# Kernel tuning notes

Measured on AMD Instinct MI355X. Metric: run time of the kernel, lower is better.

The kernel has to match this reference:

```python
import jax, jax.numpy as jnp
import numpy as np

E = 512
H = 8
D = E // H  # 64
B = 2
S = 4096


def setup_inputs() -> dict:
    key = jax.random.key(0)
    ks = jax.random.split(key, 12)
    s = 1.0 / np.sqrt(E)
    return {
        "x": jax.random.normal(ks[0], (B, S, E), dtype=jnp.float32),
        "bias": jax.random.normal(ks[1], (H, 1, S, S), dtype=jnp.float32),
        "mask": jax.random.randint(ks[2], (1, 1, S, S), 0, 2, dtype=jnp.int32),
        "Wq": jax.random.normal(ks[3], (E, E), dtype=jnp.float32) * s,
        "bq": jnp.zeros((E,), dtype=jnp.float32),
        "Wk": jax.random.normal(ks[4], (E, E), dtype=jnp.float32) * s,
        "bk": jnp.zeros((E,), dtype=jnp.float32),
        "Wv": jax.random.normal(ks[5], (E, E), dtype=jnp.float32) * s,
        "bv": jnp.zeros((E,), dtype=jnp.float32),
        "Wo": jax.random.normal(ks[6], (E, E), dtype=jnp.float32) * s,
        "bo": jnp.zeros((E,), dtype=jnp.float32),
    }


def _split_heads(t):
    # [B,S,E] -> [H,B,S,D]  (matches x.view(B,-1,H,D).permute(2,0,1,3))
    b, s, _ = t.shape
    return t.reshape(b, s, H, D).transpose(2, 0, 1, 3)


def reference(x, bias, mask, Wq, bq, Wk, bk, Wv, bv, Wo, bo):
    # torch Linear: y = x @ W.T + b
    q = _split_heads(x @ Wq.T + bq)  # [H,B,S,D]
    k = _split_heads(x @ Wk.T + bk)
    v = _split_heads(x @ Wv.T + bv)

    scores = jnp.einsum("hbqd,hbkd->hbqk", q, k) + bias  # [H,B,S,S]
    scores = jnp.where(mask == 0, jnp.float32(-1e20), scores)
    # NOTE: original divides AFTER bias-add and masking
    probs = jax.nn.softmax(scores / jnp.sqrt(jnp.float32(D)), axis=-1)
    out = jnp.einsum("hbqk,hbkd->hbqd", probs, v)  # [H,B,S,D]
    out = out.transpose(1, 2, 0, 3).reshape(x.shape[0], -1, H * D)  # [B,S,E]
    return out @ Wo.T + bo
```

## Files before the change

kernel.cpp:

```cpp
#include <hip/hip_runtime.h>
#include <hip/hip_bf16.h>

typedef __bf16 bf16x8 __attribute__((ext_vector_type(8)));
typedef float f32x4 __attribute__((ext_vector_type(4)));

#define S_LEN 4096
#define EMB   512
#define NHEAD 8
#define HDIM  64
#define NBAT  2
#define NROW  (NBAT * S_LEN)

static __device__ __forceinline__ f32x4 mfma16x16(bf16x8 a, bf16x8 b, f32x4 c) {
    return __builtin_amdgcn_mfma_f32_16x16x32_bf16(a, b, c, 0, 0, 0);
}

__global__ __launch_bounds__(256) void convert_kernel(
    const float* __restrict__ x, const float* __restrict__ Wq,
    const float* __restrict__ Wk, const float* __restrict__ Wv,
    const float* __restrict__ Wo,
    __hip_bfloat16* __restrict__ xb, __hip_bfloat16* __restrict__ wqkv,
    __hip_bfloat16* __restrict__ wob)
{
    const int NX = NROW * EMB;
    const int NW = EMB * EMB;
    int i = blockIdx.x * 256 + threadIdx.x;
    if (i < NX) { xb[i] = __float2bfloat16(x[i]); return; }
    int j = i - NX;
    if (j < 3 * NW) {
        int p = j >> 18, r = j & (NW - 1);
        const float* src = (p == 0) ? Wq : (p == 1) ? Wk : Wv;
        wqkv[j] = __float2bfloat16(src[r]);
    } else if (j < 4 * NW) {
        int r = j - 3 * NW;
        wob[r] = __float2bfloat16(Wo[r]);
    }
}

__device__ __forceinline__ void gemm_core(
    const __hip_bfloat16* __restrict__ A, const __hip_bfloat16* __restrict__ Bw,
    int mbase, int nbase,
    __hip_bfloat16* As, __hip_bfloat16* Bs, f32x4 acc[2][4])
{
    const int tid = threadIdx.x;
    const int w = tid >> 6, lane = tid & 63, l = lane & 15, quad = lane >> 4;
    const f32x4 zero = {0.f, 0.f, 0.f, 0.f};
#pragma unroll
    for (int mb = 0; mb < 2; mb++)
#pragma unroll
        for (int nb = 0; nb < 4; nb++) acc[mb][nb] = zero;

    for (int k0 = 0; k0 < EMB; k0 += 32) {
        __syncthreads();
#pragma unroll
        for (int c = tid; c < 512; c += 256) {
            int row = c >> 2, kc = c & 3;
            uint4 v = *(const uint4*)(A + (size_t)(mbase + row) * EMB + k0 + kc * 8);
            *(uint4*)(As + row * 40 + kc * 8) = v;
        }
        {
            int row = tid >> 2, kc = tid & 3;
            uint4 v = *(const uint4*)(Bw + (size_t)(nbase + row) * EMB + k0 + kc * 8);
            *(uint4*)(Bs + row * 40 + kc * 8) = v;
        }
        __syncthreads();

        bf16x8 af[2], bfr[4];
#pragma unroll
        for (int mb = 0; mb < 2; mb++)
            af[mb] = *(const bf16x8*)(As + (w * 32 + mb * 16 + l) * 40 + quad * 8);
#pragma unroll
        for (int nb = 0; nb < 4; nb++)
            bfr[nb] = *(const bf16x8*)(Bs + (nb * 16 + l) * 40 + quad * 8);
#pragma unroll
        for (int mb = 0; mb < 2; mb++)
#pragma unroll
            for (int nb = 0; nb < 4; nb++)
                acc[mb][nb] = mfma16x16(af[mb], bfr[nb], acc[mb][nb]);
    }
}

__global__ __launch_bounds__(256, 4) void qkv_gemm(
    const __hip_bfloat16* __restrict__ xb, const __hip_bfloat16* __restrict__ wqkv,
    const float* __restrict__ bq, const float* __restrict__ bk, const float* __restrict__ bv,
    __hip_bfloat16* __restrict__ Qh, __hip_bfloat16* __restrict__ Kh,
    __hip_bfloat16* __restrict__ Vt)
{
    __shared__ __align__(16) __hip_bfloat16 As[128 * 40];
    __shared__ __align__(16) __hip_bfloat16 Bs[64 * 40];
    const int mbase = blockIdx.x * 128, nbase = blockIdx.y * 64;
    f32x4 acc[2][4];
    gemm_core(xb, wqkv, mbase, nbase, As, Bs, acc);

    const int tid = threadIdx.x;
    const int w = tid >> 6, lane = tid & 63, l = lane & 15, quad = lane >> 4;
    const int p = nbase >> 9;
    const float* bias = (p == 0) ? bq : (p == 1) ? bk : bv;
    __hip_bfloat16* dst = (p == 0) ? Qh : (p == 1) ? Kh : Vt;
#pragma unroll
    for (int mb = 0; mb < 2; mb++)
#pragma unroll
        for (int nb = 0; nb < 4; nb++)
#pragma unroll
            for (int r = 0; r < 4; r++) {
                int m = mbase + w * 32 + mb * 16 + quad * 4 + r;
                int n = nbase + nb * 16 + l;
                int o = n & 511;
                float v = acc[mb][nb][r] + bias[o];
                int b = m >> 12, s = m & 4095, hh = o >> 6, d = o & 63;
                size_t idx = (p == 2)
                    ? ((size_t)((hh * 2 + b) * 64 + d)) * 4096 + s
                    : ((size_t)((hh * 2 + b) * 4096 + s)) * 64 + d;
                dst[idx] = __float2bfloat16(v);
            }
}

__global__ __launch_bounds__(256, 2) void attn_kernel(
    const __hip_bfloat16* __restrict__ Qh, const __hip_bfloat16* __restrict__ Kh,
    const __hip_bfloat16* __restrict__ Vt,
    const float* __restrict__ bias, const int* __restrict__ mask,
    __hip_bfloat16* __restrict__ Om)
{
    const int h = blockIdx.y, qt = blockIdx.x;
    const int tid = threadIdx.x;
    const int w = tid >> 6, lane = tid & 63, l = lane & 15, quad = lane >> 4;
    const int q0 = qt * 64;
    const float CS = 0.18033688011112042f;

    __shared__ __align__(16) __hip_bfloat16 Ks[2][64 * 72];
    __shared__ __align__(16) __hip_bfloat16 Vs[2][64 * 72];
    __shared__ __align__(16) __hip_bfloat16 Ps[64 * 72];

    bf16x8 qf[2][2];
#pragma unroll
    for (int b = 0; b < 2; b++) {
        const __hip_bfloat16* qp =
            Qh + ((size_t)((h * 2 + b) * 4096 + q0 + w * 16 + l)) * 64;
        qf[b][0] = *(const bf16x8*)(qp + quad * 8);
        qf[b][1] = *(const bf16x8*)(qp + 32 + quad * 8);
    }

    f32x4 oacc[2][4];
    float mst[2][4], lst[2][4];
    const f32x4 zero = {0.f, 0.f, 0.f, 0.f};
#pragma unroll
    for (int b = 0; b < 2; b++) {
#pragma unroll
        for (int nb = 0; nb < 4; nb++) oacc[b][nb] = zero;
#pragma unroll
        for (int r = 0; r < 4; r++) { mst[b][r] = -__builtin_inff(); lst[b][r] = 0.f; }
    }

    for (int kt = 0; kt < 64; kt++) {
        const int k0 = kt * 64;
        __syncthreads();
#pragma unroll
        for (int c = tid; c < 2048; c += 256) {
            int t = c >> 9;
            int b = t & 1, isV = t >> 1;
            int cc = c & 511, row = cc >> 3, ch = cc & 7;
            const __hip_bfloat16* src = isV
                ? Vt + ((size_t)((h * 2 + b) * 64 + row)) * 4096 + k0 + ch * 8
                : Kh + ((size_t)((h * 2 + b) * 4096 + k0 + row)) * 64 + ch * 8;
            uint4 v = *(const uint4*)src;
            *(uint4*)((isV ? Vs[b] : Ks[b]) + row * 72 + ch * 8) = v;
        }
        float bor[4][4];
#pragma unroll
        for (int nb = 0; nb < 4; nb++)
#pragma unroll
            for (int r = 0; r < 4; r++) {
                int qq = q0 + w * 16 + quad * 4 + r;
                int kk = k0 + nb * 16 + l;
                float bb = bias[(size_t)h * S_LEN * S_LEN + (size_t)qq * S_LEN + kk];
                int mm = mask[(size_t)qq * S_LEN + kk];
                bor[nb][r] = mm ? bb : -1e30f;
            }
        __syncthreads();

#pragma unroll
        for (int b = 0; b < 2; b++) {
            f32x4 sc[4] = {zero, zero, zero, zero};
#pragma unroll
            for (int ks = 0; ks < 2; ks++)
#pragma unroll
                for (int nb = 0; nb < 4; nb++) {
                    bf16x8 kf = *(const bf16x8*)(Ks[b] + (nb * 16 + l) * 72 + ks * 32 + quad * 8);
                    sc[nb] = mfma16x16(qf[b][ks], kf, sc[nb]);
                }
            float xv[4][4], rmax[4];
#pragma unroll
            for (int r = 0; r < 4; r++) rmax[r] = -__builtin_inff();
#pragma unroll
            for (int nb = 0; nb < 4; nb++)
#pragma unroll
                for (int r = 0; r < 4; r++) {
                    xv[nb][r] = (sc[nb][r] + bor[nb][r]) * CS;
                    rmax[r] = fmaxf(rmax[r], xv[nb][r]);
                }
#pragma unroll
            for (int r = 0; r < 4; r++) {
                rmax[r] = fmaxf(rmax[r], __shfl_xor(rmax[r], 1));
                rmax[r] = fmaxf(rmax[r], __shfl_xor(rmax[r], 2));
                rmax[r] = fmaxf(rmax[r], __shfl_xor(rmax[r], 4));
                rmax[r] = fmaxf(rmax[r], __shfl_xor(rmax[r], 8));
            }
            float alpha[4], rsum[4];
#pragma unroll
            for (int r = 0; r < 4; r++) {
                float mn = fmaxf(mst[b][r], rmax[r]);
                alpha[r] = __builtin_amdgcn_exp2f(mst[b][r] - mn);
                mst[b][r] = mn;
                rsum[r] = 0.f;
            }
            float pv[4][4];
#pragma unroll
            for (int nb = 0; nb < 4; nb++)
#pragma unroll
                for (int r = 0; r < 4; r++) {
                    float e = __builtin_amdgcn_exp2f(xv[nb][r] - mst[b][r]);
                    pv[nb][r] = e;
                    rsum[r] += e;
                }
#pragma unroll
            for (int r = 0; r < 4; r++) {
                rsum[r] += __shfl_xor(rsum[r], 1);
                rsum[r] += __shfl_xor(rsum[r], 2);
                rsum[r] += __shfl_xor(rsum[r], 4);
                rsum[r] += __shfl_xor(rsum[r], 8);
                lst[b][r] = lst[b][r] * alpha[r] + rsum[r];
            }
#pragma unroll
            for (int nb = 0; nb < 4; nb++)
#pragma unroll
                for (int r = 0; r < 4; r++) oacc[b][nb][r] *= alpha[r];
#pragma unroll
            for (int nb = 0; nb < 4; nb++)
#pragma unroll
                for (int r = 0; r < 4; r++)
                    Ps[(w * 16 + quad * 4 + r) * 72 + nb * 16 + l] =
                        __float2bfloat16(pv[nb][r]);
#pragma unroll
            for (int ks = 0; ks < 2; ks++) {
                bf16x8 pf = *(const bf16x8*)(Ps + (w * 16 + l) * 72 + ks * 32 + quad * 8);
#pragma unroll
                for (int nb = 0; nb < 4; nb++) {
                    bf16x8 vf = *(const bf16x8*)(Vs[b] + (nb * 16 + l) * 72 + ks * 32 + quad * 8);
                    oacc[b][nb] = mfma16x16(pf, vf, oacc[b][nb]);
                }
            }
        }
    }

#pragma unroll
    for (int b = 0; b < 2; b++)
#pragma unroll
        for (int nb = 0; nb < 4; nb++)
#pragma unroll
            for (int r = 0; r < 4; r++) {
                int qq = q0 + w * 16 + quad * 4 + r;
                float val = oacc[b][nb][r] / lst[b][r];
                Om[((size_t)(b * 4096 + qq)) * 512 + h * 64 + nb * 16 + l] =
                    __float2bfloat16(val);
            }
}

__global__ __launch_bounds__(256, 4) void out_gemm(
    const __hip_bfloat16* __restrict__ Om, const __hip_bfloat16* __restrict__ wob,
    const float* __restrict__ bo, float* __restrict__ out)
{
    __shared__ __align__(16) __hip_bfloat16 As[128 * 40];
    __shared__ __align__(16) __hip_bfloat16 Bs[64 * 40];
    const int mbase = blockIdx.x * 128, nbase = blockIdx.y * 64;
    f32x4 acc[2][4];
    gemm_core(Om, wob, mbase, nbase, As, Bs, acc);

    const int tid = threadIdx.x;
    const int w = tid >> 6, lane = tid & 63, l = lane & 15, quad = lane >> 4;
#pragma unroll
    for (int mb = 0; mb < 2; mb++)
#pragma unroll
        for (int nb = 0; nb < 4; nb++)
#pragma unroll
            for (int r = 0; r < 4; r++) {
                int m = mbase + w * 32 + mb * 16 + quad * 4 + r;
                int n = nbase + nb * 16 + l;
                out[(size_t)m * EMB + n] = acc[mb][nb][r] + bo[n];
            }
}

extern "C" void kernel_launch(void* const* d_in, const int* in_sizes, int n_in,
                              void* d_out, int out_size, void* d_ws, size_t ws_size,
                              hipStream_t stream) {
    const float* x    = (const float*)d_in[0];
    const float* bias = (const float*)d_in[1];
    const int*   mask = (const int*)d_in[2];
    const float* Wq   = (const float*)d_in[3];
    const float* bq   = (const float*)d_in[4];
    const float* Wk   = (const float*)d_in[5];
    const float* bk   = (const float*)d_in[6];
    const float* Wv   = (const float*)d_in[7];
    const float* bv   = (const float*)d_in[8];
    const float* Wo   = (const float*)d_in[9];
    const float* bo   = (const float*)d_in[10];
    float* out = (float*)d_out;

    char* ws = (char*)d_ws;
    __hip_bfloat16* xb   = (__hip_bfloat16*)ws; ws += (size_t)NROW * EMB * 2;
    __hip_bfloat16* wqkv = (__hip_bfloat16*)ws; ws += (size_t)3 * EMB * EMB * 2;
    __hip_bfloat16* wob  = (__hip_bfloat16*)ws; ws += (size_t)EMB * EMB * 2;
    __hip_bfloat16* Qh   = (__hip_bfloat16*)ws; ws += (size_t)NROW * EMB * 2;
    __hip_bfloat16* Kh   = (__hip_bfloat16*)ws; ws += (size_t)NROW * EMB * 2;
    __hip_bfloat16* Vt   = (__hip_bfloat16*)ws; ws += (size_t)NROW * EMB * 2;
    __hip_bfloat16* Om   = (__hip_bfloat16*)ws; ws += (size_t)NROW * EMB * 2;

    convert_kernel<<<dim3(20480), dim3(256), 0, stream>>>(
        x, Wq, Wk, Wv, Wo, xb, wqkv, wob);
    qkv_gemm<<<dim3(64, 24), dim3(256), 0, stream>>>(
        xb, wqkv, bq, bk, bv, Qh, Kh, Vt);
    attn_kernel<<<dim3(64, NHEAD), dim3(256), 0, stream>>>(
        Qh, Kh, Vt, bias, mask, Om);
    out_gemm<<<dim3(64, 8), dim3(256), 0, stream>>>(Om, wob, bo, out);
}
```

Measured before the change: 1.316 ms.

## Prefetch next K/V, bias and mask tiles into registers and raise MFMA priority

Result: faster. 1.261 ms (-4.1%).

```diff
diff --git a/kernel.cpp b/kernel.cpp
--- a/kernel.cpp
+++ b/kernel.cpp
@@ -50,21 +50,26 @@
 #pragma unroll
         for (int nb = 0; nb < 4; nb++) acc[mb][nb] = zero;
 
+    const int r0 = tid >> 2, kc = tid & 3;
+    const __hip_bfloat16* pa0 = A + (size_t)(mbase + r0) * EMB + kc * 8;
+    const __hip_bfloat16* pa1 = pa0 + (size_t)64 * EMB;
+    const __hip_bfloat16* pb  = Bw + (size_t)(nbase + r0) * EMB + kc * 8;
+
+    uint4 va0 = *(const uint4*)pa0;
+    uint4 va1 = *(const uint4*)pa1;
+    uint4 vb  = *(const uint4*)pb;
+
     for (int k0 = 0; k0 < EMB; k0 += 32) {
         __syncthreads();
-#pragma unroll
-        for (int c = tid; c < 512; c += 256) {
-            int row = c >> 2, kc = c & 3;
-            uint4 v = *(const uint4*)(A + (size_t)(mbase + row) * EMB + k0 + kc * 8);
-            *(uint4*)(As + row * 40 + kc * 8) = v;
-        }
-        {
-            int row = tid >> 2, kc = tid & 3;
-            uint4 v = *(const uint4*)(Bw + (size_t)(nbase + row) * EMB + k0 + kc * 8);
-            *(uint4*)(Bs + row * 40 + kc * 8) = v;
-        }
+        *(uint4*)(As + r0 * 40 + kc * 8)        = va0;
+        *(uint4*)(As + (r0 + 64) * 40 + kc * 8) = va1;
+        *(uint4*)(Bs + r0 * 40 + kc * 8)        = vb;
         __syncthreads();
-
+        if (k0 + 32 < EMB) {
+            va0 = *(const uint4*)(pa0 + k0 + 32);
+            va1 = *(const uint4*)(pa1 + k0 + 32);
+            vb  = *(const uint4*)(pb  + k0 + 32);
+        }
         bf16x8 af[2], bfr[4];
 #pragma unroll
         for (int mb = 0; mb < 2; mb++)
@@ -72,11 +77,13 @@
 #pragma unroll
         for (int nb = 0; nb < 4; nb++)
             bfr[nb] = *(const bf16x8*)(Bs + (nb * 16 + l) * 40 + quad * 8);
+        __builtin_amdgcn_s_setprio(1);
 #pragma unroll
         for (int mb = 0; mb < 2; mb++)
 #pragma unroll
             for (int nb = 0; nb < 4; nb++)
                 acc[mb][nb] = mfma16x16(af[mb], bfr[nb], acc[mb][nb]);
+        __builtin_amdgcn_s_setprio(0);
     }
 }
 
@@ -121,7 +128,7 @@
     const float* __restrict__ bias, const int* __restrict__ mask,
     __hip_bfloat16* __restrict__ Om)
 {
-    const int h = blockIdx.y, qt = blockIdx.x;
+    const int h = blockIdx.x, qt = blockIdx.y;
     const int tid = threadIdx.x;
     const int w = tid >> 6, lane = tid & 63, l = lane & 15, quad = lane >> 4;
     const int q0 = qt * 64;
@@ -151,36 +158,81 @@
         for (int r = 0; r < 4; r++) { mst[b][r] = -__builtin_inff(); lst[b][r] = 0.f; }
     }
 
+    const __hip_bfloat16* kvsrc[8];
+    __hip_bfloat16* kvdst[8];
+#pragma unroll
+    for (int j = 0; j < 8; j++) {
+        int c = j * 256 + tid;
+        int t = c >> 9, b = t & 1, isV = t >> 1;
+        int cc = c & 511, row = cc >> 3, ch = cc & 7;
+        if (isV) {
+            kvsrc[j] = Vt + ((size_t)((h * 2 + b) * 64 + row)) * 4096 + ch * 8;
+            kvdst[j] = Vs[b] + row * 72 + ch * 8;
+        } else {
+            kvsrc[j] = Kh + ((size_t)((h * 2 + b) * 4096 + row)) * 64 + ch * 8;
+            kvdst[j] = Ks[b] + row * 72 + ch * 8;
+        }
+    }
+    const float* bptr[4];
+    const int*   mptr[4];
+#pragma unroll
+    for (int r = 0; r < 4; r++) {
+        int qq = q0 + w * 16 + quad * 4 + r;
+        bptr[r] = bias + (size_t)h * S_LEN * S_LEN + (size_t)qq * S_LEN + l;
+        mptr[r] = mask + (size_t)qq * S_LEN + l;
+    }
+
+    uint4 kvbuf[8];
+    float bb[4][4];
+    int   mm[4][4];
+#pragma unroll
+    for (int j = 0; j < 8; j++) {
+        kvbuf[j] = *(const uint4*)kvsrc[j];
+        kvsrc[j] += (j >> 2) ? 64 : 64 * 64;
+    }
+#pragma unroll
+    for (int nb = 0; nb < 4; nb++)
+#pragma unroll
+        for (int r = 0; r < 4; r++) {
+            bb[nb][r] = bptr[r][nb * 16];
+            mm[nb][r] = mptr[r][nb * 16];
+        }
+#pragma unroll
+    for (int r = 0; r < 4; r++) { bptr[r] += 64; mptr[r] += 64; }
+
     for (int kt = 0; kt < 64; kt++) {
-        const int k0 = kt * 64;
         __syncthreads();
 #pragma unroll
-        for (int c = tid; c < 2048; c += 256) {
-            int t = c >> 9;
-            int b = t & 1, isV = t >> 1;
-            int cc = c & 511, row = cc >> 3, ch = cc & 7;
-            const __hip_bfloat16* src = isV
-                ? Vt + ((size_t)((h * 2 + b) * 64 + row)) * 4096 + k0 + ch * 8
-                : Kh + ((size_t)((h * 2 + b) * 4096 + k0 + row)) * 64 + ch * 8;
-            uint4 v = *(const uint4*)src;
-            *(uint4*)((isV ? Vs[b] : Ks[b]) + row * 72 + ch * 8) = v;
-        }
+        for (int j = 0; j < 8; j++) *(uint4*)kvdst[j] = kvbuf[j];
         float bor[4][4];
 #pragma unroll
         for (int nb = 0; nb < 4; nb++)
 #pragma unroll
-            for (int r = 0; r < 4; r++) {
-                int qq = q0 + w * 16 + quad * 4 + r;
-                int kk = k0 + nb * 16 + l;
-                float bb = bias[(size_t)h * S_LEN * S_LEN + (size_t)qq * S_LEN + kk];
-                int mm = mask[(size_t)qq * S_LEN + kk];
-                bor[nb][r] = mm ? bb : -1e30f;
-            }
+            for (int r = 0; r < 4; r++)
+                bor[nb][r] = mm[nb][r] ? bb[nb][r] : -1e30f;
         __syncthreads();
+
+        if (kt < 63) {
+#pragma unroll
+            for (int j = 0; j < 8; j++) {
+                kvbuf[j] = *(const uint4*)kvsrc[j];
+                kvsrc[j] += (j >> 2) ? 64 : 64 * 64;
+            }
+#pragma unroll
+            for (int nb = 0; nb < 4; nb++)
+#pragma unroll
+                for (int r = 0; r < 4; r++) {
+                    bb[nb][r] = bptr[r][nb * 16];
+                    mm[nb][r] = mptr[r][nb * 16];
+                }
+#pragma unroll
+            for (int r = 0; r < 4; r++) { bptr[r] += 64; mptr[r] += 64; }
+        }
 
 #pragma unroll
         for (int b = 0; b < 2; b++) {
             f32x4 sc[4] = {zero, zero, zero, zero};
+            __builtin_amdgcn_s_setprio(1);
 #pragma unroll
             for (int ks = 0; ks < 2; ks++)
 #pragma unroll
@@ -188,6 +240,7 @@
                     bf16x8 kf = *(const bf16x8*)(Ks[b] + (nb * 16 + l) * 72 + ks * 32 + quad * 8);
                     sc[nb] = mfma16x16(qf[b][ks], kf, sc[nb]);
                 }
+            __builtin_amdgcn_s_setprio(0);
             float xv[4][4], rmax[4];
 #pragma unroll
             for (int r = 0; r < 4; r++) rmax[r] = -__builtin_inff();
@@ -213,14 +266,14 @@
                 mst[b][r] = mn;
                 rsum[r] = 0.f;
             }
-            float pv[4][4];
 #pragma unroll
             for (int nb = 0; nb < 4; nb++)
 #pragma unroll
                 for (int r = 0; r < 4; r++) {
                     float e = __builtin_amdgcn_exp2f(xv[nb][r] - mst[b][r]);
-                    pv[nb][r] = e;
                     rsum[r] += e;
+                    Ps[(w * 16 + quad * 4 + r) * 72 + nb * 16 + l] =
+                        __float2bfloat16(e);
                 }
 #pragma unroll
             for (int r = 0; r < 4; r++) {
@@ -234,12 +287,7 @@
             for (int nb = 0; nb < 4; nb++)
 #pragma unroll
                 for (int r = 0; r < 4; r++) oacc[b][nb][r] *= alpha[r];
-#pragma unroll
-            for (int nb = 0; nb < 4; nb++)
-#pragma unroll
-                for (int r = 0; r < 4; r++)
-                    Ps[(w * 16 + quad * 4 + r) * 72 + nb * 16 + l] =
-                        __float2bfloat16(pv[nb][r]);
+            __builtin_amdgcn_s_setprio(1);
 #pragma unroll
             for (int ks = 0; ks < 2; ks++) {
                 bf16x8 pf = *(const bf16x8*)(Ps + (w * 16 + l) * 72 + ks * 32 + quad * 8);
@@ -249,6 +297,7 @@
                     oacc[b][nb] = mfma16x16(pf, vf, oacc[b][nb]);
                 }
             }
+            __builtin_amdgcn_s_setprio(0);
         }
     }
 
@@ -318,7 +367,7 @@
         x, Wq, Wk, Wv, Wo, xb, wqkv, wob);
     qkv_gemm<<<dim3(64, 24), dim3(256), 0, stream>>>(
         xb, wqkv, bq, bk, bv, Qh, Kh, Vt);
-    attn_kernel<<<dim3(64, NHEAD), dim3(256), 0, stream>>>(
+    attn_kernel<<<dim3(NHEAD, 64), dim3(256), 0, stream>>>(
         Qh, Kh, Vt, bias, mask, Om);
     out_gemm<<<dim3(64, 8), dim3(256), 0, stream>>>(Om, wob, bo, out);
 }
```
